# Performance work log

Measured on AMD Instinct MI355X. Metric: run time of the kernel, lower is better.

Reference implementation:

```python
import jax, jax.numpy as jnp
import numpy as np

N_NODES = 7823
N_DRUG = 708
N_TARGET = 1512
N_DISEASE = N_NODES - N_DRUG - N_TARGET  # 5603
FEAT = 1024
HID = 512
OUT = 256
LN_EPS = 1e-5


def _adapter_params(key, in_dim, out_dim):
    k1, k2 = jax.random.split(key)
    s1 = (2.0 / (in_dim + out_dim)) ** 0.5
    return dict(
        W=jax.random.normal(k1, (out_dim, in_dim), jnp.float32) * s1,
        b=jnp.zeros((out_dim,), jnp.float32),
        g=jnp.ones((out_dim,), jnp.float32),
        beta=jnp.zeros((out_dim,), jnp.float32),
        Wr=jax.random.normal(k2, (out_dim, in_dim), jnp.float32) * s1,
        br=jnp.zeros((out_dim,), jnp.float32),
    )


def setup_inputs() -> dict:
    key = jax.random.key(0)
    ks = jax.random.split(key, 12)
    inp = {
        'drug_feats': jax.random.normal(ks[0], (N_DRUG, FEAT), jnp.float32),
        'target_feats': jax.random.normal(ks[1], (N_TARGET, FEAT), jnp.float32),
        'disease_feats': jax.random.normal(ks[2], (N_DISEASE, FEAT), jnp.float32),
        'drug_adjs': jax.random.uniform(ks[3], (2, N_NODES, N_NODES), jnp.float32),
        'target_adjs': jax.random.uniform(ks[4], (2, N_NODES, N_NODES), jnp.float32),
    }
    # adapters
    for name, k in [('dA', ks[5]), ('tA', ks[6]), ('sA', ks[7])]:
        p = _adapter_params(k, FEAT, HID)
        for pn, pv in p.items():
            inp[name + '_' + pn] = pv
    # GCN weights: gc1 [HID,OUT], gc2 [OUT,OUT], uniform(-1/sqrt(out),1/sqrt(out))
    stdv = 1.0 / (OUT ** 0.5)
    inp['dG_W1'] = jax.random.uniform(ks[8], (HID, OUT), jnp.float32, -stdv, stdv)
    inp['dG_W2'] = jax.random.uniform(ks[9], (OUT, OUT), jnp.float32, -stdv, stdv)
    inp['tG_W1'] = jax.random.uniform(ks[10], (HID, OUT), jnp.float32, -stdv, stdv)
    inp['tG_W2'] = jax.random.uniform(ks[11], (OUT, OUT), jnp.float32, -stdv, stdv)
    inp['dG_a'] = jnp.full((1,), 0.25, jnp.float32)  # PReLU init
    inp['tG_a'] = jnp.full((1,), 0.25, jnp.float32)
    return inp


def _layernorm(x, g, b):
    m = x.mean(-1, keepdims=True)
    v = x.var(-1, keepdims=True)
    return (x - m) / jnp.sqrt(v + LN_EPS) * g + b


def _adapter(x, W, b, g, beta, Wr, br):
    out = jax.nn.relu(_layernorm(x @ W.T + b, g, beta))
    return out + x @ Wr.T + br


def _prelu(x, a):
    return jnp.where(x >= 0, x, a * x)


def _gcn(x, adj, W1, W2, a):
    h = _prelu(adj @ (x @ W1), a)
    Z = adj @ (h @ W2)
    # nn.LayerNorm(Z.size()) normalizes over the WHOLE tensor, no affine
    return (Z - Z.mean()) / jnp.sqrt(Z.var() + LN_EPS)


def reference(drug_feats, target_feats, disease_feats, drug_adjs, target_adjs,
              dA_W, dA_b, dA_g, dA_beta, dA_Wr, dA_br,
              tA_W, tA_b, tA_g, tA_beta, tA_Wr, tA_br,
              sA_W, sA_b, sA_g, sA_beta, sA_Wr, sA_br,
              dG_W1, dG_W2, dG_a, tG_W1, tG_W2, tG_a):
    h_drug = jax.nn.elu(_adapter(drug_feats, dA_W, dA_b, dA_g, dA_beta, dA_Wr, dA_br))
    h_target = jax.nn.elu(_adapter(target_feats, tA_W, tA_b, tA_g, tA_beta, tA_Wr, tA_br))
    h_disease = jax.nn.elu(_adapter(disease_feats, sA_W, sA_b, sA_g, sA_beta, sA_Wr, sA_br))
    x_all = jnp.concatenate([h_drug, h_target, h_disease], axis=0)  # [7823, HID]
    adj_d = drug_adjs.mean(0)
    adj_t = target_adjs.mean(0)
    z_drug = _gcn(x_all, adj_d, dG_W1, dG_W2, dG_a)[:N_DRUG]
    z_target = _gcn(x_all, adj_t, tG_W1, tG_W2, tG_a)[N_DRUG:N_DRUG + N_TARGET]
    z_drug = z_drug / (jnp.linalg.norm(z_drug, axis=1, keepdims=True) + 1e-8)
    z_target = z_target / (jnp.linalg.norm(z_target, axis=1, keepdims=True) + 1e-8)
    return (z_drug, z_target)
```

## Files before the change

### kernel.cpp

```cpp
#include <hip/hip_runtime.h>
#include <hip/hip_bf16.h>
#include <stdint.h>

typedef __attribute__((ext_vector_type(8))) short short8;
typedef __attribute__((ext_vector_type(4))) float f32x4;

#define N_DRUG 708
#define N_TGT  1512
#define N_NODES 7823
#define N_D_T  2220
#define KPAD   8192
#define MROWP  7936
#define NTOT   2002688
#define NSPLIT 4
#define PLANE  61199329LL
#define ADJSTR ((long long)MROWP*KPAD)
#define BTSTR  ((long long)256*KPAD)
#define PSTR   ((long long)NSPLIT*NTOT)

__device__ __forceinline__ unsigned short f2bf(float f) {
  union { float f; unsigned int i; } v; v.f = f;
  unsigned int r = v.i + 0x7FFF + ((v.i >> 16) & 1);
  return (unsigned short)(r >> 16);
}

__device__ __forceinline__ int4 pack8(const float v[8]) {
  union { int4 i4; unsigned short u[8]; } r;
  #pragma unroll
  for (int j = 0; j < 8; j++) r.u[j] = f2bf(v[j]);
  return r.i4;
}


__global__ __launch_bounds__(256) void cast_wc(
    const float* __restrict__ w0, const float* __restrict__ wr0,
    const float* __restrict__ w1, const float* __restrict__ wr1,
    const float* __restrict__ w2, const float* __restrict__ wr2,
    unsigned short* __restrict__ Wc)
{
  long long i4 = ((long long)blockIdx.x*256 + threadIdx.x)*4;
  int g  = (int)(i4 >> 20);
  int rr = (int)((i4 >> 10) & 1023);
  int c  = (int)(i4 & 1023);
  const float* src = (g==0) ? (rr<512?w0:wr0) : (g==1) ? (rr<512?w1:wr1) : (rr<512?w2:wr2);
  float4 f = *(const float4*)(src + (long long)(rr & 511)*1024 + c);
  ushort4 v; v.x=f2bf(f.x); v.y=f2bf(f.y); v.z=f2bf(f.z); v.w=f2bf(f.w);
  *(ushort4*)&Wc[i4] = v;
}

__global__ __launch_bounds__(256) void transpose_cast(
    const float* __restrict__ src, unsigned short* __restrict__ dst, int R, int C)
{
  int i = blockIdx.x*256 + threadIdx.x;
  if (i >= R*C) return;
  int r = i / C, c = i - r*C;
  dst[c*R + r] = f2bf(src[i]);
}

__global__ __launch_bounds__(256) void mean_cast_row(
    const float* __restrict__ A0, const float* __restrict__ A1,
    unsigned short* __restrict__ D)
{
  int row = blockIdx.x;
  const float* p0 = (blockIdx.y ? A1 : A0) + (long long)row*N_NODES;
  const float* p1 = p0 + PLANE;
  unsigned short* d = D + (long long)blockIdx.y*ADJSTR + (long long)row*KPAD;

  for (int c = threadIdx.x*8; c < 7816; c += 2048) {
    float4 a0 = *(const float4*)(p0+c);
    float4 a1 = *(const float4*)(p0+c+4);
    float4 b0 = *(const float4*)(p1+c);
    float4 b1 = *(const float4*)(p1+c+4);
    float v[8] = {0.5f*(a0.x+b0.x), 0.5f*(a0.y+b0.y), 0.5f*(a0.z+b0.z), 0.5f*(a0.w+b0.w),
                  0.5f*(a1.x+b1.x), 0.5f*(a1.y+b1.y), 0.5f*(a1.z+b1.z), 0.5f*(a1.w+b1.w)};
    *(int4*)(d + c) = pack8(v);
  }
  int t = threadIdx.x;
  if (t < 7) {
    int c = 7816 + t;
    d[c] = f2bf(0.5f*(p0[c] + p1[c]));
  }
}

__global__ __launch_bounds__(512, 2) void spmmK(
    const unsigned short* __restrict__ Abase,
    const unsigned short* __restrict__ Bbase,
    float* __restrict__ parts)
{
  __shared__ __align__(16) unsigned short Bs[2][256*128];

  int bid = (blockIdx.x & 7)*62 + (blockIdx.x >> 3);
  int grp = bid / 62;
  int mt  = bid % 62;
  int b  = grp >> 2;
  int ks = grp & 3;

  const unsigned short* A  = Abase + b*ADJSTR;
  const unsigned short* BT = Bbase + b*BTSTR;
  int m0 = mt*128;
  int kt0 = ks*32;

  int tid = threadIdx.x, lane = tid & 63, w = tid >> 6;
  int wm = (w>>1)*32, wn = (w&1)*128;
  int grow = m0 + wm + (lane&15);
  long long rA0 = (long long)grow*KPAD + (lane>>4)*8;

  f32x4 acc[2][8] = {};

  int srow[8], sslot[8];
  #pragma unroll
  for (int i=0;i<8;i++){ int c = i*512 + tid; srow[i] = c>>4; sslot[i] = c&15; }

  int4 bregA[8], bregB[8];
  auto loadB = [&](int sub, int4* br){
    long long kb = (long long)kt0*64 + sub*128;
    #pragma unroll
    for (int i=0;i<8;i++)
      br[i] = *(const int4*)(BT + (long long)srow[i]*KPAD + kb + sslot[i]*8);
  };
  auto storeB = [&](unsigned short* buf, const int4* br){
    #pragma unroll
    for (int i=0;i<8;i++)
      *(int4*)(buf + srow[i]*128 + (sslot[i]^(srow[i]&7))*8) = br[i];
  };
  auto loadA = [&](int g, int4* a){
    const unsigned short* p = A + rA0 + (long long)g*64;
    a[0] = *(const int4*)(p);
    a[1] = *(const int4*)(p + 16*KPAD);
    a[2] = *(const int4*)(p + 32);
    a[3] = *(const int4*)(p + 16*KPAD + 32);
  };
  auto compute = [&](int lt, const int4* a, const unsigned short* buf){
    #pragma unroll
    for (int kk=0; kk<2; ++kk) {
      short8 bv[8];
      #pragma unroll
      for (int nf=0; nf<8; ++nf) {
        int row = wn + nf*16 + (lane&15);
        int sl  = (lt*8 + kk*4 + (lane>>4)) ^ (lane&7);
        bv[nf] = *(const short8*)&buf[row*128 + sl*8];
      }
      #pragma unroll
      for (int mf=0; mf<2; ++mf) {
        short8 av = *(const short8*)&a[kk*2+mf];
        #pragma unroll
        for (int nf=0; nf<8; ++nf)
          acc[mf][nf] = __builtin_amdgcn_mfma_f32_16x16x32_bf16(av, bv[nf], acc[mf][nf], 0, 0, 0);
      }
    }
  };

  int gmax = kt0 + 31;
  int4 a0[4], a1[4], a2[4], a3[4];

  loadB(0, bregA);
  loadA(kt0+0, a0);
  loadA(kt0+1, a1);
  loadA(kt0+2, a2);
  loadA(kt0+3, a3);
  storeB(&Bs[0][0], bregA);
  loadB(1, bregA);
  loadB(2, bregB);
  asm volatile("s_waitcnt lgkmcnt(0)" ::: "memory");
  __builtin_amdgcn_s_barrier();
  __builtin_amdgcn_sched_barrier(0);

  int cur = 0;
  #pragma unroll 1
  for (int sp = 0; sp < 8; ++sp) {
    int g = kt0 + sp*4;
    {
      const unsigned short* Bc = &Bs[cur][0];
      compute(0, a0, Bc); loadA(min(g+4, gmax), a0);
      compute(1, a1, Bc); loadA(min(g+5, gmax), a1);
      __builtin_amdgcn_s_barrier();
      __builtin_amdgcn_sched_barrier(0);
      storeB(&Bs[cur^1][0], bregA);
      loadB(min(2*sp+3, 15), bregA);
      asm volatile("s_waitcnt lgkmcnt(0)" ::: "memory");
      __builtin_amdgcn_s_barrier();
      __builtin_amdgcn_sched_barrier(0);
      cur ^= 1;
    }
    {
      const unsigned short* Bc = &Bs[cur][0];
      compute(0, a2, Bc); loadA(min(g+6, gmax), a2);
      compute(1, a3, Bc); loadA(min(g+7, gmax), a3);
      if (sp < 7) {
        __builtin_amdgcn_s_barrier();
        __builtin_amdgcn_sched_barrier(0);
        storeB(&Bs[cur^1][0], bregB);
        loadB(min(2*sp+4, 15), bregB);
        asm volatile("s_waitcnt lgkmcnt(0)" ::: "memory");
        __builtin_amdgcn_s_barrier();
        __builtin_amdgcn_sched_barrier(0);
        cur ^= 1;
      }
    }
  }

  float* P = parts + b*PSTR + (long long)ks*NTOT;
  #pragma unroll
  for (int mf=0; mf<2; ++mf) {
    int mb = m0 + wm + mf*16 + ((lane>>4)<<2);
    #pragma unroll
    for (int i=0;i<4;i++){
      int m = mb + i;
      if (m < N_NODES) {
        #pragma unroll
        for (int nf=0; nf<8; ++nf) {
          int n = wn + nf*16 + (lane&15);
          P[(long long)m*256 + n] = acc[mf][nf][i];
        }
      }
    }
  }
}

#define BN 256
#define BK 64

__global__ __launch_bounds__(512, 4) void gemmS(
    const unsigned short* __restrict__ Abase, long long a_bstr, int lda,
    const unsigned short* __restrict__ Bbase, long long b_bstr, int ldb,
    int m_cnt, int tiles_m, int ktiles,
    unsigned short* __restrict__ CTb, long long ct_bstr, int ldct)
{
  __shared__ __align__(16) unsigned short As[64*BK];
  __shared__ __align__(16) unsigned short Bs[BN*BK];

  int bid = blockIdx.x;
  int b   = bid / tiles_m;
  int tm  = bid % tiles_m;

  const unsigned short* A  = Abase + b*a_bstr;
  const unsigned short* BT = Bbase + b*b_bstr;

  int m0 = tm*64;
  int tid = threadIdx.x;
  int lane = tid & 63, w = tid >> 6;
  int wm = (w >> 2)*32, wn = (w & 3)*64;

  f32x4 acc[2][4] = {};

  int arow, aslot, brow[4], bslot[4];
  { int c = tid; arow = c>>3; aslot = c&7; }
  #pragma unroll
  for (int i=0;i<4;i++){ int c = i*512 + tid; brow[i] = c>>3; bslot[i] = c&7; }

  int4 ra, rb[4];
  auto loadAB = [&](int kt){
    int gr = m0 + arow; if (gr > m_cnt-1) gr = m_cnt-1;
    ra = *(const int4*)(A + (long long)gr*lda + kt*BK + aslot*8);
    #pragma unroll
    for (int i=0;i<4;i++)
      rb[i] = *(const int4*)(BT + (long long)brow[i]*ldb + kt*BK + bslot[i]*8);
  };
  auto storeAB = [&](){
    *(int4*)(As + arow*BK + (aslot^(arow&7))*8) = ra;
    #pragma unroll
    for (int i=0;i<4;i++)
      *(int4*)(Bs + brow[i]*BK + (bslot[i]^(brow[i]&7))*8) = rb[i];
  };

  loadAB(0);
  for (int kt = 0; kt < ktiles; ++kt) {
    __syncthreads();
    storeAB();
    __syncthreads();
    if (kt+1 < ktiles) loadAB(kt+1);
    #pragma unroll
    for (int kk=0; kk<2; ++kk) {
      short8 av[2], bv[4];
      #pragma unroll
      for (int x=0;x<2;x++){
        int row = wm + x*16 + (lane&15);
        int slot = kk*4 + (lane>>4);
        av[x] = *(const short8*)&As[row*BK + (slot^(row&7))*8];
      }
      #pragma unroll
      for (int x=0;x<4;x++){
        int row = wn + x*16 + (lane&15);
        int slot = kk*4 + (lane>>4);
        bv[x] = *(const short8*)&Bs[row*BK + (slot^(row&7))*8];
      }
      #pragma unroll
      for (int mf=0; mf<2; ++mf)
        #pragma unroll
        for (int nf=0; nf<4; ++nf)
          acc[mf][nf] = __builtin_amdgcn_mfma_f32_16x16x32_bf16(av[mf], bv[nf], acc[mf][nf], 0, 0, 0);
    }
  }

  unsigned short* CT = CTb + b*ct_bstr;
  #pragma unroll
  for (int nf=0; nf<4; ++nf) {
    int n = wn + nf*16 + (lane&15);
    #pragma unroll
    for (int mf=0; mf<2; ++mf) {
      int mb = m0 + wm + mf*16 + ((lane>>4)<<2);
      ushort4 v;
      v.x = (mb+0 < m_cnt) ? f2bf(acc[mf][nf][0]) : (unsigned short)0;
      v.y = (mb+1 < m_cnt) ? f2bf(acc[mf][nf][1]) : (unsigned short)0;
      v.z = (mb+2 < m_cnt) ? f2bf(acc[mf][nf][2]) : (unsigned short)0;
      v.w = (mb+3 < m_cnt) ? f2bf(acc[mf][nf][3]) : (unsigned short)0;
      *(ushort4*)&CT[(long long)n*ldct + mb] = v;
    }
  }
}

__global__ __launch_bounds__(512, 4) void adapt_gemm(
    const float* __restrict__ f0, const float* __restrict__ f1, const float* __restrict__ f2,
    const unsigned short* __restrict__ Wc, float* __restrict__ C1)
{
  __shared__ __align__(16) unsigned short As[64*BK];
  __shared__ __align__(16) unsigned short Bs[BN*BK];

  int bid = blockIdx.x;
  int tn = bid & 3, tq = bid >> 2;
  int g, lt, m_cnt, gstart;
  if (tq < 12)      { g=0; lt=tq;    m_cnt=N_DRUG;           gstart=0; }
  else if (tq < 36) { g=1; lt=tq-12; m_cnt=N_TGT;            gstart=N_DRUG; }
  else              { g=2; lt=tq-36; m_cnt=N_NODES-N_D_T;    gstart=N_D_T; }
  const float* A = (g==0) ? f0 : (g==1) ? f1 : f2;
  const unsigned short* BT = Wc + (long long)g*1024*1024;

  int m0 = lt*64, n0 = tn*BN;
  int tid = threadIdx.x;
  int lane = tid & 63, w = tid >> 6;
  int wm = (w >> 2)*32, wn = (w & 3)*64;

  f32x4 acc[2][4] = {};

  int arow, aslot, brow[4], bslot[4];
  { int c = tid; arow = c>>3; aslot = c&7; }
  #pragma unroll
  for (int i=0;i<4;i++){ int c = i*512 + tid; brow[i] = c>>3; bslot[i] = c&7; }

  int4 ra, rb[4];
  auto loadAB = [&](int kt){
    int gr = m0 + arow; if (gr > m_cnt-1) gr = m_cnt-1;
    const float* p = A + (long long)gr*1024 + kt*BK + aslot*8;
    float4 q0 = *(const float4*)p;
    float4 q1 = *(const float4*)(p+4);
    float v[8] = {q0.x,q0.y,q0.z,q0.w,q1.x,q1.y,q1.z,q1.w};
    ra = pack8(v);
    #pragma unroll
    for (int i=0;i<4;i++)
      rb[i] = *(const int4*)(BT + (long long)(n0 + brow[i])*1024 + kt*BK + bslot[i]*8);
  };
  auto storeAB = [&](){
    *(int4*)(As + arow*BK + (aslot^(arow&7))*8) = ra;
    #pragma unroll
    for (int i=0;i<4;i++)
      *(int4*)(Bs + brow[i]*BK + (bslot[i]^(brow[i]&7))*8) = rb[i];
  };

  loadAB(0);
  for (int kt = 0; kt < 16; ++kt) {
    __syncthreads();
    storeAB();
    __syncthreads();
    if (kt+1 < 16) loadAB(kt+1);
    #pragma unroll
    for (int kk=0; kk<2; ++kk) {
      short8 av[2], bv[4];
      #pragma unroll
      for (int x=0;x<2;x++){
        int row = wm + x*16 + (lane&15);
        int slot = kk*4 + (lane>>4);
        av[x] = *(const short8*)&As[row*BK + (slot^(row&7))*8];
      }
      #pragma unroll
      for (int x=0;x<4;x++){
        int row = wn + x*16 + (lane&15);
        int slot = kk*4 + (lane>>4);
        bv[x] = *(const short8*)&Bs[row*BK + (slot^(row&7))*8];
      }
      #pragma unroll
      for (int mf=0; mf<2; ++mf)
        #pragma unroll
        for (int nf=0; nf<4; ++nf)
          acc[mf][nf] = __builtin_amdgcn_mfma_f32_16x16x32_bf16(av[mf], bv[nf], acc[mf][nf], 0, 0, 0);
    }
  }

  #pragma unroll
  for (int mf=0; mf<2; ++mf) {
    int mb = m0 + wm + mf*16 + ((lane>>4)<<2);
    #pragma unroll
    for (int i=0;i<4;i++){
      int m = mb + i;
      if (m < m_cnt) {
        #pragma unroll
        for (int nf=0; nf<4; ++nf) {
          int n = n0 + wn + nf*16 + (lane&15);
          C1[(long long)(gstart+m)*1024 + n] = acc[mf][nf][i];
        }
      }
    }
  }
}


__global__ __launch_bounds__(256) void adapter_fuse(
    const float* __restrict__ C1,
    const float* __restrict__ b0, const float* __restrict__ g0, const float* __restrict__ be0, const float* __restrict__ br0,
    const float* __restrict__ b1, const float* __restrict__ g1, const float* __restrict__ be1, const float* __restrict__ br1,
    const float* __restrict__ b2, const float* __restrict__ g2, const float* __restrict__ be2, const float* __restrict__ br2,
    unsigned short* __restrict__ xall)
{
  int r = blockIdx.x;
  const float *b, *g, *be, *br;
  if (r < N_DRUG)     { b=b0; g=g0; be=be0; br=br0; }
  else if (r < N_D_T) { b=b1; g=g1; be=be1; br=br1; }
  else                { b=b2; g=g2; be=be2; br=br2; }
  int t = threadIdx.x;
  const float* row = C1 + (long long)r*1024;
  float ya = row[t]       + b[t];
  float yb = row[t + 256] + b[t + 256];
  float s = ya + yb, q = ya*ya + yb*yb;
  #pragma unroll
  for (int o=32;o;o>>=1){ s += __shfl_down(s,o); q += __shfl_down(q,o); }
  __shared__ float ss[4], qq[4];
  if ((t & 63) == 0) { ss[t>>6]=s; qq[t>>6]=q; }
  __syncthreads();
  float S = ss[0]+ss[1]+ss[2]+ss[3];
  float Q = qq[0]+qq[1]+qq[2]+qq[3];
  float mean = S * (1.f/512.f);
  float var  = Q * (1.f/512.f) - mean*mean;
  float inv  = rsqrtf(var + 1e-5f);
  float za = fmaxf((ya-mean)*inv*g[t]     + be[t],     0.f);
  float zb = fmaxf((yb-mean)*inv*g[t+256] + be[t+256], 0.f);
  float ha = za + row[512 + t] + br[t];
  float hb = zb + row[768 + t] + br[t + 256];
  ha = (ha > 0.f) ? ha : (expf(ha) - 1.f);
  hb = (hb > 0.f) ? hb : (expf(hb) - 1.f);
  xall[(long long)r*512 + t]       = f2bf(ha);
  xall[(long long)r*512 + t + 256] = f2bf(hb);
}

__global__ __launch_bounds__(256) void reduce_prelu2(
    const float* __restrict__ parts, const float* __restrict__ a0, const float* __restrict__ a1,
    unsigned short* __restrict__ h)
{
  int b = blockIdx.y;
  long long i = (long long)blockIdx.x*256 + threadIdx.x;
  const float* P = parts + b*PSTR;
  float s = 0.f;
  #pragma unroll
  for (int p=0;p<NSPLIT;p++) s += P[(long long)p*NTOT + i];
  float a = (b ? a1 : a0)[0];
  h[b*(long long)NTOT + i] = f2bf(s >= 0.f ? s : a*s);
}

__global__ __launch_bounds__(256) void reduce_stats2(
    const float* __restrict__ parts, float* __restrict__ Z, float* __restrict__ sp)
{
  int b = blockIdx.y;
  long long i = (long long)blockIdx.x*256 + threadIdx.x;
  const float* P = parts + b*PSTR;
  float s = 0.f;
  #pragma unroll
  for (int p=0;p<NSPLIT;p++) s += P[(long long)p*NTOT + i];
  Z[b*(long long)NTOT + i] = s;
  float a = s, q = s*s;
  #pragma unroll
  for (int o=32;o;o>>=1){ a += __shfl_down(a,o); q += __shfl_down(q,o); }
  __shared__ float ss[4], qq[4];
  int t = threadIdx.x;
  if ((t&63)==0){ ss[t>>6]=a; qq[t>>6]=q; }
  __syncthreads();
  if (t==0) {
    sp[(long long)b*2*N_NODES + 2*blockIdx.x]   = ss[0]+ss[1]+ss[2]+ss[3];
    sp[(long long)b*2*N_NODES + 2*blockIdx.x+1] = qq[0]+qq[1]+qq[2]+qq[3];
  }
}

__global__ __launch_bounds__(256) void stats_final2(
    const float* __restrict__ sp, float* __restrict__ stats)
{
  int b = blockIdx.x;
  const float* S = sp + (long long)b*2*N_NODES;
  int t = threadIdx.x;
  float s = 0.f, q = 0.f;
  for (int i=t; i<N_NODES; i+=256){ s += S[2*i]; q += S[2*i+1]; }
  #pragma unroll
  for (int o=32;o;o>>=1){ s += __shfl_down(s,o); q += __shfl_down(q,o); }
  __shared__ float ss[4], qq[4];
  if ((t&63)==0){ ss[t>>6]=s; qq[t>>6]=q; }
  __syncthreads();
  if (t==0){ stats[b*16]=ss[0]+ss[1]+ss[2]+ss[3]; stats[b*16+1]=qq[0]+qq[1]+qq[2]+qq[3]; }
}

__global__ __launch_bounds__(256) void finalize(
    const float* __restrict__ Z, const float* __restrict__ stats,
    float* __restrict__ out, int row_lo, long long out_off)
{
  int r = row_lo + blockIdx.x;
  int t = threadIdx.x;
  float mean = stats[0] * (1.f/(float)NTOT);
  float var  = stats[1] * (1.f/(float)NTOT) - mean*mean;
  float inv  = rsqrtf(var + 1e-5f);
  float z = (Z[(long long)r*256 + t] - mean) * inv;
  float q = z*z;
  #pragma unroll
  for (int o=32;o;o>>=1) q += __shfl_down(q,o);
  __shared__ float qq[4];
  if ((t&63)==0) qq[t>>6]=q;
  __syncthreads();
  float norm = sqrtf(qq[0]+qq[1]+qq[2]+qq[3]);
  out[out_off + (long long)blockIdx.x*256 + t] = z / (norm + 1e-8f);
}


extern "C" void kernel_launch(void* const* d_in, const int* in_sizes, int n_in,
                              void* d_out, int out_size, void* d_ws, size_t ws_size,
                              hipStream_t stream)
{
  const float* drug_feats    = (const float*)d_in[0];
  const float* target_feats  = (const float*)d_in[1];
  const float* disease_feats = (const float*)d_in[2];
  const float* drug_adjs     = (const float*)d_in[3];
  const float* target_adjs   = (const float*)d_in[4];
  const float* dA_W  = (const float*)d_in[5];
  const float* dA_b  = (const float*)d_in[6];
  const float* dA_g  = (const float*)d_in[7];
  const float* dA_be = (const float*)d_in[8];
  const float* dA_Wr = (const float*)d_in[9];
  const float* dA_br = (const float*)d_in[10];
  const float* tA_W  = (const float*)d_in[11];
  const float* tA_b  = (const float*)d_in[12];
  const float* tA_g  = (const float*)d_in[13];
  const float* tA_be = (const float*)d_in[14];
  const float* tA_Wr = (const float*)d_in[15];
  const float* tA_br = (const float*)d_in[16];
  const float* sA_W  = (const float*)d_in[17];
  const float* sA_b  = (const float*)d_in[18];
  const float* sA_g  = (const float*)d_in[19];
  const float* sA_be = (const float*)d_in[20];
  const float* sA_Wr = (const float*)d_in[21];
  const float* sA_br = (const float*)d_in[22];
  const float* dG_W1 = (const float*)d_in[23];
  const float* dG_W2 = (const float*)d_in[24];
  const float* tG_W1 = (const float*)d_in[25];
  const float* tG_W2 = (const float*)d_in[26];
  const float* dG_a  = (const float*)d_in[27];
  const float* tG_a  = (const float*)d_in[28];

  char* ws = (char*)d_ws;
  size_t off = 0;
  auto alloc = [&](size_t bytes)->void* {
    void* p = ws + off;
    off += (bytes + 255) & ~(size_t)255;
    return p;
  };

  unsigned short* Wc   = (unsigned short*)alloc((size_t)3*1024*1024*2);
  unsigned short* W1T  = (unsigned short*)alloc((size_t)2*256*512*2);
  unsigned short* W2T  = (unsigned short*)alloc((size_t)2*256*256*2);
  unsigned short* xall = (unsigned short*)alloc((size_t)N_NODES*512*2);
  unsigned short* adjb = (unsigned short*)alloc((size_t)2*ADJSTR*2);
  unsigned short* xw1T = (unsigned short*)alloc((size_t)2*BTSTR*2);
  unsigned short* hbuf = (unsigned short*)alloc((size_t)2*NTOT*2);
  unsigned short* hw2T = (unsigned short*)alloc((size_t)2*BTSTR*2);
  float* parts = (float*)alloc((size_t)2*PSTR*4);
  float* Zf    = (float*)alloc((size_t)2*NTOT*4);
  float* spart = (float*)alloc((size_t)2*N_NODES*2*4);
  float* stats = (float*)alloc((size_t)32*4);
  float* C1    = parts;
  float* outp  = (float*)d_out;

  cast_wc<<<3072, 256, 0, stream>>>(dA_W, dA_Wr, tA_W, tA_Wr, sA_W, sA_Wr, Wc);
  transpose_cast<<<512, 256, 0, stream>>>(dG_W1, W1T,            512, 256);
  transpose_cast<<<512, 256, 0, stream>>>(tG_W1, W1T + 256*512,  512, 256);
  transpose_cast<<<256, 256, 0, stream>>>(dG_W2, W2T,            256, 256);
  transpose_cast<<<256, 256, 0, stream>>>(tG_W2, W2T + 256*256,  256, 256);

  adapt_gemm<<<496, 512, 0, stream>>>(drug_feats, target_feats, disease_feats, Wc, C1);
  adapter_fuse<<<N_NODES, 256, 0, stream>>>(C1,
      dA_b, dA_g, dA_be, dA_br,
      tA_b, tA_g, tA_be, tA_br,
      sA_b, sA_g, sA_be, sA_br, xall);

  gemmS<<<2*128, 512, 0, stream>>>(
      xall, 0, 512, W1T, 256*512, 512,
      N_NODES, 128, 8, xw1T, BTSTR, KPAD);

  mean_cast_row<<<dim3(N_NODES, 2), 256, 0, stream>>>(drug_adjs, target_adjs, adjb);

  spmmK<<<496, 512, 0, stream>>>(adjb, xw1T, parts);

  reduce_prelu2<<<dim3(N_NODES,2), 256, 0, stream>>>(parts, dG_a, tG_a, hbuf);

  gemmS<<<2*128, 512, 0, stream>>>(
      hbuf, (long long)NTOT, 256, W2T, 256*256, 256,
      N_NODES, 128, 4, hw2T, BTSTR, KPAD);

  spmmK<<<496, 512, 0, stream>>>(adjb, hw2T, parts);

  reduce_stats2<<<dim3(N_NODES,2), 256, 0, stream>>>(parts, Zf, spart);
  stats_final2<<<2, 256, 0, stream>>>(spart, stats);

  finalize<<<N_DRUG, 256, 0, stream>>>(Zf, stats, outp, 0, 0LL);
  finalize<<<N_TGT, 256, 0, stream>>>(Zf + NTOT, stats + 16, outp, N_DRUG, (long long)N_DRUG*256);
}
```

Before: 1.025 ms.

## Split spmm N dimension into two 128-wide tiles to raise occupancy

The dense adjacency-times-features kernel now tiles N at 128 instead of 256. This halves the LDS B buffer and accumulator registers, which permits four blocks per CU and doubles the grid to 992 blocks. The B prefetch moves from two register sets to a single one. The cost is that each A (adjacency) tile is now read twice, once per N half, which doubles global traffic on the large bf16 adjacency matrix.

After: 1.227 ms. +19.7%, slower.

```diff
diff --git a/kernel.cpp b/kernel.cpp
--- a/kernel.cpp
+++ b/kernel.cpp
@@ -82,46 +82,47 @@
   }
 }
 
-__global__ __launch_bounds__(512, 2) void spmmK(
+__global__ __launch_bounds__(512, 4) void spmmK(
     const unsigned short* __restrict__ Abase,
     const unsigned short* __restrict__ Bbase,
     float* __restrict__ parts)
 {
-  __shared__ __align__(16) unsigned short Bs[2][256*128];
-
-  int bid = (blockIdx.x & 7)*62 + (blockIdx.x >> 3);
-  int grp = bid / 62;
-  int mt  = bid % 62;
+  __shared__ __align__(16) unsigned short Bs[2][128*128];
+
+  int bid = (blockIdx.x & 7)*124 + (blockIdx.x >> 3);
+  int grp = bid / 124;
+  int q   = bid % 124;
   int b  = grp >> 2;
   int ks = grp & 3;
+  int mt = q >> 1, nt = q & 1;
 
   const unsigned short* A  = Abase + b*ADJSTR;
   const unsigned short* BT = Bbase + b*BTSTR;
-  int m0 = mt*128;
+  int m0 = mt*128, n0 = nt*128;
   int kt0 = ks*32;
 
   int tid = threadIdx.x, lane = tid & 63, w = tid >> 6;
-  int wm = (w>>1)*32, wn = (w&1)*128;
+  int wm = (w>>1)*32, wn = (w&1)*64;
   int grow = m0 + wm + (lane&15);
   long long rA0 = (long long)grow*KPAD + (lane>>4)*8;
 
-  f32x4 acc[2][8] = {};
-
-  int srow[8], sslot[8];
-  #pragma unroll
-  for (int i=0;i<8;i++){ int c = i*512 + tid; srow[i] = c>>4; sslot[i] = c&15; }
-
-  int4 bregA[8], bregB[8];
-  auto loadB = [&](int sub, int4* br){
+  f32x4 acc[2][4] = {};
+
+  int srow[4], sslot[4];
+  #pragma unroll
+  for (int i=0;i<4;i++){ int c = i*512 + tid; srow[i] = c>>4; sslot[i] = c&15; }
+
+  int4 breg[4];
+  auto loadB = [&](int sub){
     long long kb = (long long)kt0*64 + sub*128;
     #pragma unroll
-    for (int i=0;i<8;i++)
-      br[i] = *(const int4*)(BT + (long long)srow[i]*KPAD + kb + sslot[i]*8);
-  };
-  auto storeB = [&](unsigned short* buf, const int4* br){
-    #pragma unroll
-    for (int i=0;i<8;i++)
-      *(int4*)(buf + srow[i]*128 + (sslot[i]^(srow[i]&7))*8) = br[i];
+    for (int i=0;i<4;i++)
+      breg[i] = *(const int4*)(BT + (long long)(n0+srow[i])*KPAD + kb + sslot[i]*8);
+  };
+  auto storeB = [&](unsigned short* buf){
+    #pragma unroll
+    for (int i=0;i<4;i++)
+      *(int4*)(buf + srow[i]*128 + (sslot[i]^(srow[i]&7))*8) = breg[i];
   };
   auto loadA = [&](int g, int4* a){
     const unsigned short* p = A + rA0 + (long long)g*64;
@@ -133,9 +134,9 @@
   auto compute = [&](int lt, const int4* a, const unsigned short* buf){
     #pragma unroll
     for (int kk=0; kk<2; ++kk) {
-      short8 bv[8];
-      #pragma unroll
-      for (int nf=0; nf<8; ++nf) {
+      short8 bv[4];
+      #pragma unroll
+      for (int nf=0; nf<4; ++nf) {
         int row = wn + nf*16 + (lane&15);
         int sl  = (lt*8 + kk*4 + (lane>>4)) ^ (lane&7);
         bv[nf] = *(const short8*)&buf[row*128 + sl*8];
@@ -144,7 +145,7 @@
       for (int mf=0; mf<2; ++mf) {
         short8 av = *(const short8*)&a[kk*2+mf];
         #pragma unroll
-        for (int nf=0; nf<8; ++nf)
+        for (int nf=0; nf<4; ++nf)
           acc[mf][nf] = __builtin_amdgcn_mfma_f32_16x16x32_bf16(av, bv[nf], acc[mf][nf], 0, 0, 0);
       }
     }
@@ -153,14 +154,13 @@
   int gmax = kt0 + 31;
   int4 a0[4], a1[4], a2[4], a3[4];
 
-  loadB(0, bregA);
+  loadB(0);
   loadA(kt0+0, a0);
   loadA(kt0+1, a1);
   loadA(kt0+2, a2);
   loadA(kt0+3, a3);
-  storeB(&Bs[0][0], bregA);
-  loadB(1, bregA);
-  loadB(2, bregB);
+  storeB(&Bs[0][0]);
+  loadB(1);
   asm volatile("s_waitcnt lgkmcnt(0)" ::: "memory");
   __builtin_amdgcn_s_barrier();
   __builtin_amdgcn_sched_barrier(0);
@@ -175,8 +175,8 @@
       compute(1, a1, Bc); loadA(min(g+5, gmax), a1);
       __builtin_amdgcn_s_barrier();
       __builtin_amdgcn_sched_barrier(0);
-      storeB(&Bs[cur^1][0], bregA);
-      loadB(min(2*sp+3, 15), bregA);
+      storeB(&Bs[cur^1][0]);
+      loadB(min(2*sp+2, 15));
       asm volatile("s_waitcnt lgkmcnt(0)" ::: "memory");
       __builtin_amdgcn_s_barrier();
       __builtin_amdgcn_sched_barrier(0);
@@ -189,8 +189,8 @@
       if (sp < 7) {
         __builtin_amdgcn_s_barrier();
         __builtin_amdgcn_sched_barrier(0);
-        storeB(&Bs[cur^1][0], bregB);
-        loadB(min(2*sp+4, 15), bregB);
+        storeB(&Bs[cur^1][0]);
+        loadB(min(2*sp+3, 15));
         asm volatile("s_waitcnt lgkmcnt(0)" ::: "memory");
         __builtin_amdgcn_s_barrier();
         __builtin_amdgcn_sched_barrier(0);
@@ -208,8 +208,8 @@
       int m = mb + i;
       if (m < N_NODES) {
         #pragma unroll
-        for (int nf=0; nf<8; ++nf) {
-          int n = wn + nf*16 + (lane&15);
+        for (int nf=0; nf<4; ++nf) {
+          int n = n0 + wn + nf*16 + (lane&15);
           P[(long long)m*256 + n] = acc[mf][nf][i];
         }
       }
@@ -589,7 +589,7 @@
 
   mean_cast_row<<<dim3(N_NODES, 2), 256, 0, stream>>>(drug_adjs, target_adjs, adjb);
 
-  spmmK<<<496, 512, 0, stream>>>(adjb, xw1T, parts);
+  spmmK<<<992, 512, 0, stream>>>(adjb, xw1T, parts);
 
   reduce_prelu2<<<dim3(N_NODES,2), 256, 0, stream>>>(parts, dG_a, tG_a, hbuf);
 
@@ -597,7 +597,7 @@
       hbuf, (long long)NTOT, 256, W2T, 256*256, 256,
       N_NODES, 128, 4, hw2T, BTSTR, KPAD);
 
-  spmmK<<<496, 512, 0, stream>>>(adjb, hw2T, parts);
+  spmmK<<<992, 512, 0, stream>>>(adjb, hw2T, parts);
 
   reduce_stats2<<<dim3(N_NODES,2), 256, 0, stream>>>(parts, Zf, spart);
   stats_final2<<<2, 256, 0, stream>>>(spart, stats);
```
